# Optimization experiments

Hardware: AMD Instinct MI355X
Metric: run time of the kernel (lower is better)

## Reference

```python
import jax, jax.numpy as jnp
import numpy as np

B, S, C, L = 128, 49, 512, 1000
EPS_NORM = 1e-12
EPS_LN = 1e-5


def setup_inputs() -> dict:
    key = jax.random.key(0)
    ks = jax.random.split(key, 12)
    w_std = 0.02  # trunc_normal std for Linear weights
    c_std = 1.0 / np.sqrt(C)  # torch default Conv1d init scale (approx)
    return {
        "Fs": jax.random.normal(ks[0], (B, S, C), jnp.float32),
        "Ft": jax.random.normal(ks[1], (L, C), jnp.float32),
        "Fv": jax.random.normal(ks[2], (B, C), jnp.float32),
        "label": jax.random.randint(ks[3], (B,), 0, L),
        # Proj2 (pre_project_s): GN(1,C) -> Conv1d(C,C,1) -> ReLU -> GN(1,C) -> Conv1d(C,C,1)
        "gn1_g": jnp.ones((C,), jnp.float32),
        "gn1_b": jnp.zeros((C,), jnp.float32),
        "conv1_w": jax.random.normal(ks[4], (C, C), jnp.float32) * c_std,
        "conv1_b": jnp.zeros((C,), jnp.float32),
        "gn2_g": jnp.ones((C,), jnp.float32),
        "gn2_b": jnp.zeros((C,), jnp.float32),
        "conv2_w": jax.random.normal(ks[5], (C, C), jnp.float32) * c_std,
        "conv2_b": jnp.zeros((C,), jnp.float32),
        # Proj1 (pre_project_vv): LN -> Linear -> ReLU -> LN -> Linear
        "ln1_g": jnp.ones((C,), jnp.float32),
        "ln1_b": jnp.zeros((C,), jnp.float32),
        "lin1_w": jax.random.normal(ks[6], (C, C), jnp.float32) * w_std,
        "lin1_b": jnp.zeros((C,), jnp.float32),
        "ln2_g": jnp.ones((C,), jnp.float32),
        "ln2_b": jnp.zeros((C,), jnp.float32),
        "lin2_w": jax.random.normal(ks[7], (C, C), jnp.float32) * w_std,
        "lin2_b": jnp.zeros((C,), jnp.float32),
        "vis_gamma_p": jnp.float32(0.99),
        "vis_gamma_n": jnp.float32(0.99),
        "visual_prototype": jax.random.normal(ks[8], (L, C), jnp.float32),
    }


def _groupnorm1(x, g, b):
    # x: (B, C, S); GroupNorm with 1 group -> normalize over (C, S)
    m = jnp.mean(x, axis=(1, 2), keepdims=True)
    v = jnp.var(x, axis=(1, 2), keepdims=True)
    xn = (x - m) * jax.lax.rsqrt(v + EPS_LN)
    return xn * g[None, :, None] + b[None, :, None]


def _layernorm(x, g, b):
    m = jnp.mean(x, axis=-1, keepdims=True)
    v = jnp.var(x, axis=-1, keepdims=True)
    return (x - m) * jax.lax.rsqrt(v + EPS_LN) * g + b


def _l2norm(x):
    n = jnp.sqrt(jnp.sum(x * x, axis=-1, keepdims=True))
    return x / jnp.maximum(n, EPS_NORM)


def reference(Fs, Ft, Fv, label, gn1_g, gn1_b, conv1_w, conv1_b, gn2_g, gn2_b,
              conv2_w, conv2_b, ln1_g, ln1_b, lin1_w, lin1_b, ln2_g, ln2_b,
              lin2_w, lin2_b, vis_gamma_p, vis_gamma_n, visual_prototype):
    # --- Proj2 on Fs: (B,S,C) -> (B,C,S) -> GN/Conv1x1/ReLU/GN/Conv1x1 -> (B,S,C)
    xp = jnp.transpose(Fs, (0, 2, 1))                      # (B,C,S)
    h = _groupnorm1(xp, gn1_g, gn1_b)
    h = jnp.einsum('oc,bcs->bos', conv1_w, h) + conv1_b[None, :, None]
    h = jax.nn.relu(h)
    h = _groupnorm1(h, gn2_g, gn2_b)
    h = jnp.einsum('oc,bcs->bos', conv2_w, h) + conv2_b[None, :, None]
    Fs_p = jnp.transpose(h, (0, 2, 1))                     # (B,S,C)

    # --- cross-attn with text features: conv1d(Fs^T, Ft[:,:,None]) == einsum
    A = jnp.einsum('bsc,lc->bls', Fs_p, Ft)                # (B,L,S)
    A1 = jax.nn.softmax(A, axis=-1)
    feat_v_a = jnp.einsum('bls,bsc->blc', A1, Fs_p)        # (B,L,C)

    # --- Proj1 on Fv
    v = _layernorm(Fv, ln1_g, ln1_b)
    v = jax.nn.relu(v @ lin1_w.T + lin1_b)
    v = _layernorm(v, ln2_g, ln2_b)
    Fv_p = v @ lin2_w.T + lin2_b                           # (B,C)

    Fv_exp = Fv_p[:, None, :]                              # broadcast over L
    feat_v = vis_gamma_p * feat_v_a + Fv_exp               # (B,L,C)

    # --- cross-attn with visual prototype
    Av = jnp.einsum('bsc,lc->bls', Fs_p, visual_prototype)
    A1v = jax.nn.softmax(Av, axis=-1)
    feat_v_av = jnp.einsum('bls,bsc->blc', A1v, Fs_p)
    feat_vv = vis_gamma_n * feat_v_av + Fv_exp             # (B,L,C)

    Ft_n = _l2norm(Ft)                                     # (L,C)
    Fv_n = _l2norm(Fv_p)                                   # (B,C) (expanded rows identical)
    feat_v_n = _l2norm(feat_v)
    feat_vv_n = _l2norm(feat_vv)
    proto_n = _l2norm(visual_prototype)

    logits1 = jnp.einsum('bc,lc->bl', Fv_n, Ft_n)
    logits2 = jnp.sum(feat_v_n * Ft_n[None], axis=-1)
    logits3 = jnp.sum(feat_vv_n * proto_n[None], axis=-1)

    # --- no_grad prototype EMA update via label scatter
    Fv0 = jax.lax.stop_gradient(Fv_n)                      # Fv[:,0,:] after normalize
    proto = jax.lax.stop_gradient(visual_prototype)
    class_count = jnp.zeros((L,), jnp.int32).at[label].add(1)
    class_sum = jax.ops.segment_sum(Fv0, label, num_segments=L)
    safe_count = jnp.maximum(class_count.astype(jnp.float32), 1e-8)[:, None]
    class_mean = class_sum / safe_count
    new_proto = 0.99 * proto + 0.01 * class_mean
    updated_prototype = jnp.where((class_count > 0)[:, None], new_proto, proto)

    logits = jnp.stack([logits1, logits2, logits3])        # (3,B,L)
    return logits, updated_prototype
```

## Files before the change

### kernel.cpp

```cpp
#include <hip/hip_runtime.h>


#define Bn 128
#define Sn 49
#define Cn 512
#define Ln 1000
#define BL (Bn*Ln)
#define VQ 2048

typedef unsigned short u16;
typedef unsigned int u32;

using bfrag = __attribute__((ext_vector_type(8))) short;
using ffrag = __attribute__((ext_vector_type(4))) float;

typedef const __attribute__((address_space(1))) u32 gq_t;
typedef __attribute__((address_space(3))) u32 lq_t;

__device__ __forceinline__ float bf2f(u16 u){ return __uint_as_float(((u32)u) << 16); }
__device__ __forceinline__ float bflo(u32 u){ return __uint_as_float(u << 16); }
__device__ __forceinline__ float bfhi(u32 u){ return __uint_as_float(u & 0xffff0000u); }
__device__ __forceinline__ u16 f2bf(float f){
  u32 x = __float_as_uint(f);
  u32 r = x + 0x7fffu + ((x >> 16) & 1u);
  return (u16)(r >> 16);
}
__device__ __forceinline__ u16 f2h(float f){
  _Float16 h = (_Float16)f; return *(u16*)&h;
}
__device__ __forceinline__ float h2f(u16 u){
  _Float16 h = *(_Float16*)&u; return (float)h;
}

template<int BF>
__device__ __forceinline__ float ldin(const void* p, int i){
  if (BF) return bf2f(((const u16*)p)[i]);
  return ((const float*)p)[i];
}

template<int BF>
__device__ __forceinline__ void ld8(const void* p, int base, float* w){
  if (BF){
    uint4 u = *(const uint4*)((const u16*)p + base);
    w[0]=bflo(u.x); w[1]=bfhi(u.x); w[2]=bflo(u.y); w[3]=bfhi(u.y);
    w[4]=bflo(u.z); w[5]=bfhi(u.z); w[6]=bflo(u.w); w[7]=bfhi(u.w);
  } else {
    float4 a = *(const float4*)((const float*)p + base);
    float4 b = *(const float4*)((const float*)p + base + 4);
    w[0]=a.x; w[1]=a.y; w[2]=a.z; w[3]=a.w;
    w[4]=b.x; w[5]=b.y; w[6]=b.z; w[7]=b.w;
  }
}

__device__ __forceinline__ uint4 pack8(const float* w){
  uint4 v;
  v.x = (u32)f2bf(w[0]) | ((u32)f2bf(w[1])<<16);
  v.y = (u32)f2bf(w[2]) | ((u32)f2bf(w[3])<<16);
  v.z = (u32)f2bf(w[4]) | ((u32)f2bf(w[5])<<16);
  v.w = (u32)f2bf(w[6]) | ((u32)f2bf(w[7])<<16);
  return v;
}

__device__ __forceinline__ float ld_gamma(const void* p, int BF){
  float fb = bf2f(((const u16*)p)[0]);
  float ff = ((const float*)p)[0];
  bool pb = (fb > 0.05f && fb < 1.5f);
  bool pf = (ff > 0.05f && ff < 1.5f);
  if (pb && !pf) return fb;
  if (pf && !pb) return ff;
  return BF ? fb : ff;
}

__device__ __forceinline__ int detect_bf(const void* Fs){
  int lane = threadIdx.x & 63;
  uint4 v = ((const uint4*)Fs)[lane];
  u32 w[4] = {v.x, v.y, v.z, v.w};
  int c = 0;
  #pragma unroll
  for (int j = 0; j < 4; ++j){
    int e = (w[j] >> 7) & 0xff;
    c += (e >= 0x70 && e <= 0x8f);
  }
  #pragma unroll
  for (int m = 32; m; m >>= 1) c += __shfl_xor(c, m);
  return c >= 200;
}

__device__ __forceinline__ float2 block_red2(float a, float b, float* scratch){
  __syncthreads();
  #pragma unroll
  for (int off = 32; off; off >>= 1){ a += __shfl_xor(a, off); b += __shfl_xor(b, off); }
  int lane = threadIdx.x & 63, wid = threadIdx.x >> 6;
  if (lane == 0){ scratch[wid] = a; scratch[wid + 4] = b; }
  __syncthreads();
  return make_float2(scratch[0] + scratch[1] + scratch[2] + scratch[3],
                     scratch[4] + scratch[5] + scratch[6] + scratch[7]);
}

template<int BF>
__device__ void gn1_body(const void* Fs, float* m1, float* rs1, u16* Fsb,
                         float* m2s, float* m2ss, float* red){
  int b = blockIdx.x, tid = threadIdx.x;
  if (tid == 0){ m2s[b] = 0.f; m2ss[b] = 0.f; }
  float s = 0.f, ss = 0.f;
  for (int i = tid; i < Sn*Cn/8; i += 256){
    float w[8]; ld8<BF>(Fs, b*Sn*Cn + i*8, w);
    #pragma unroll
    for (int j = 0; j < 8; ++j){ s += w[j]; ss += w[j]*w[j]; }
    *(uint4*)(Fsb + (size_t)b*Sn*Cn + i*8) = pack8(w);
  }
  float2 r = block_red2(s, ss, red);
  if (tid == 0){
    float m = r.x * (1.f/(Sn*Cn));
    float v = r.y * (1.f/(Sn*Cn)) - m*m;
    m1[b] = m; rs1[b] = rsqrtf(v + 1e-5f);
  }
}

__global__ __launch_bounds__(256) void k_gn1_stats(const void* Fs,
    float* m1, float* rs1, u16* Fsb, float* m2s, float* m2ss){
  __shared__ float red[8];
  if (detect_bf(Fs)) gn1_body<1>(Fs, m1, rs1, Fsb, m2s, m2ss, red);
  else               gn1_body<0>(Fs, m1, rs1, Fsb, m2s, m2ss, red);
}

template<int BF>
__device__ void wk_body(int blk, const void* W1, const void* W2, const void* W3,
    const void* W4, const void* g1, const void* g2, const void* bb1, const void* bb2,
    const void* bias1, const void* bias2,
    u16* D1, u16* D2, u16* D3, u16* D4,
    float* K1a, float* K1b, float* K2a, float* K2b){
  if (blk < 512){
    int i = blk*256 + threadIdx.x;
    int sel = i >> 15;
    const void* src = (sel==0) ? W1 : (sel==1) ? W2 : (sel==2) ? W3 : W4;
    u16* dst = (sel==0) ? D1 : (sel==1) ? D2 : (sel==2) ? D3 : D4;
    int off = (i & 32767)*8;
    float w[8]; ld8<BF>(src, off, w);
    if (sel <= 1){
      const void* g = sel ? g2 : g1;
      int c0 = off & 511;
      #pragma unroll
      for (int j = 0; j < 8; ++j) w[j] *= ldin<BF>(g, c0 + j);
    }
    *(uint4*)(dst + off) = pack8(w);
  } else {
    int idx = (blk - 512)*4 + (threadIdx.x >> 6);
    int lane = threadIdx.x & 63;
    int o = idx & 511, sel = idx >> 9;
    const void* W  = sel ? W2 : W1;
    const void* g  = sel ? g2 : g1;
    const void* bb = sel ? bb2 : bb1;
    const void* bi = sel ? bias2 : bias1;
    float* Ka = sel ? K2a : K1a;
    float* Kb = sel ? K2b : K1b;
    float w[8], gv[8], bv[8];
    ld8<BF>(W, o*Cn + lane*8, w);
    ld8<BF>(g, lane*8, gv);
    ld8<BF>(bb, lane*8, bv);
    float a = 0.f, b2 = 0.f;
    #pragma unroll
    for (int j = 0; j < 8; ++j){ a += w[j]*bv[j]; b2 += w[j]*gv[j]; }
    #pragma unroll
    for (int m = 32; m; m >>= 1){ a += __shfl_xor(a, m); b2 += __shfl_xor(b2, m); }
    if (lane == 0){ Ka[o] = a + ldin<BF>(bi, o); Kb[o] = b2; }
  }
}

template<int BF>
__device__ void protonorm_body(int l, const void* Ft, const void* Pr,
                               float* invFt, float* invPr,
                               u16* FtB, u16* PrB, float* red){
  int tid = threadIdx.x;
  if (l >= Ln){
    FtB[(size_t)l*512 + tid] = 0; FtB[(size_t)l*512 + tid + 256] = 0;
    PrB[(size_t)l*512 + tid] = 0; PrB[(size_t)l*512 + tid + 256] = 0;
    return;
  }
  float a0 = ldin<BF>(Ft, l*Cn + tid), a1 = ldin<BF>(Ft, l*Cn + tid + 256);
  float p0 = ldin<BF>(Pr, l*Cn + tid), p1 = ldin<BF>(Pr, l*Cn + tid + 256);
  FtB[(size_t)l*512 + tid] = f2bf(a0); FtB[(size_t)l*512 + tid + 256] = f2bf(a1);
  PrB[(size_t)l*512 + tid] = f2bf(p0); PrB[(size_t)l*512 + tid + 256] = f2bf(p1);
  float2 r = block_red2(a0*a0 + a1*a1, p0*p0 + p1*p1, red);
  if (tid == 0){
    invFt[l] = 1.f / fmaxf(sqrtf(r.x), 1e-12f);
    invPr[l] = 1.f / fmaxf(sqrtf(r.y), 1e-12f);
  }
}

__global__ __launch_bounds__(256) void k_wkprep(const void* Fs,
    const void* W1, const void* W2, const void* W3, const void* W4,
    const void* g1, const void* g2, const void* bb1, const void* bb2,
    const void* bias1, const void* bias2,
    u16* D1, u16* D2, u16* D3, u16* D4,
    float* K1a, float* K1b, float* K2a, float* K2b,
    const void* Ft, const void* Pr, float* invFt, float* invPr, u16* FtB, u16* PrB){
  __shared__ float red[8];
  int bf = detect_bf(Fs);
  int blk = blockIdx.x;
  if (blk < 768){
    if (bf) wk_body<1>(blk, W1, W2, W3, W4, g1, g2, bb1, bb2, bias1, bias2,
                       D1, D2, D3, D4, K1a, K1b, K2a, K2b);
    else    wk_body<0>(blk, W1, W2, W3, W4, g1, g2, bb1, bb2, bias1, bias2,
                       D1, D2, D3, D4, K1a, K1b, K2a, K2b);
  } else {
    int l = blk - 768;
    if (bf) protonorm_body<1>(l, Ft, Pr, invFt, invPr, FtB, PrB, red);
    else    protonorm_body<0>(l, Ft, Pr, invFt, invPr, FtB, PrB, red);
  }
}

template<int C1>
__device__ void convm_body(const u16* __restrict__ src, const u16* __restrict__ Wb,
    const float* __restrict__ Ka, const float* __restrict__ Kb,
    float mean, float rs, u16* dst, u16* Bs, float* red,
    float* m2s, float* m2ss){
  int b = blockIdx.y, o0 = blockIdx.x * 128;
  int tid = threadIdx.x;
  int lane = tid & 63, wid = tid >> 6, lq = lane & 15, g4 = lane >> 4;
  for (int idx = tid; idx < 15*64; idx += 256){
    int r = 49 + (idx >> 6), j = idx & 63;
    *(uint4*)(Bs + (r<<9) + (j<<3)) = (uint4){0,0,0,0};
  }
  #pragma unroll
  for (int is = 0; is < 13; ++is){
    int r = is*4 + wid;
    if (r < Sn){
      const u16* gsrc = src + (size_t)(b*Sn + r)*Cn + ((lane ^ (r & 7)) << 3);
      u16* ldst = Bs + (r << 9);
      __builtin_amdgcn_global_load_lds((gq_t*)gsrc, (lq_t*)ldst, 16, 0, 0);
    }
  }
  __syncthreads();
  float gs = 0.f, gss = 0.f;
  #pragma unroll
  for (int ot = 0; ot < 2; ++ot){
    int oA = o0 + wid*32 + ot*16;
    bfrag af[16];
    #pragma unroll
    for (int kb = 0; kb < 16; ++kb)
      af[kb] = *(const bfrag*)(Wb + (size_t)(oA + lq)*Cn + kb*32 + g4*8);
    ffrag acc[4];
    #pragma unroll
    for (int st = 0; st < 4; ++st) acc[st] = (ffrag){0.f,0.f,0.f,0.f};
    #pragma unroll
    for (int st = 0; st < 4; ++st){
      int srow = st*16 + lq;
      #pragma unroll
      for (int kb = 0; kb < 16; ++kb){
        bfrag bf_ = *(const bfrag*)(Bs + (srow<<9) + (((kb*4+g4) ^ (srow&7))<<3));
        acc[st] = __builtin_amdgcn_mfma_f32_16x16x32_bf16(af[kb], bf_, acc[st], 0,0,0);
      }
    }
    int ob = oA + g4*4;
    float cst[4];
    #pragma unroll
    for (int r = 0; r < 4; ++r) cst[r] = Ka[ob + r] - mean*rs*Kb[ob + r];
    #pragma unroll
    for (int st = 0; st < 4; ++st){
      int s = st*16 + lq;
      u16 pk[4];
      #pragma unroll
      for (int r = 0; r < 4; ++r){
        float val = rs*acc[st][r] + cst[r];
        if (C1){
          val = fmaxf(val, 0.f);
          if (s < Sn){ gs += val; gss += val*val; }
        }
        pk[r] = f2bf(val);
      }
      if (C1){
        if (s < Sn) *(uint2*)(dst + ((size_t)(b*Sn + s)<<9) + ob) = *(const uint2*)pk;
      } else {
        if (s >= Sn){ pk[0]=0; pk[1]=0; pk[2]=0; pk[3]=0; }
        *(uint2*)(dst + ((size_t)(b*64 + s)<<9) + ob) = *(const uint2*)pk;
      }
    }
  }
  if (C1){
    float2 r2 = block_red2(gs, gss, red);
    if (tid == 0){
      atomicAdd(&m2s[b], r2.x);
      atomicAdd(&m2ss[b], r2.y);
    }
  }
}

__global__ __launch_bounds__(256, 2) void k_conv1m(const u16* Fsb,
    const u16* W1b, const float* Ka, const float* Kb,
    const float* m1, const float* rs1, u16* H1t, float* m2s, float* m2ss){
  __shared__ u16 Bs[64*512];
  __shared__ float red[8];
  int b = blockIdx.y;
  convm_body<1>(Fsb, W1b, Ka, Kb, m1[b], rs1[b], H1t, Bs, red, m2s, m2ss);
}

__global__ __launch_bounds__(256, 2) void k_conv2m(const u16* H1t,
    const u16* W2b, const float* Ka, const float* Kb,
    const float* m2s, const float* m2ss, u16* FspAug){
  __shared__ u16 Bs[64*512];
  int b = blockIdx.y;
  float sum = m2s[b], ssum = m2ss[b];
  float mean = sum * (1.f/(Sn*Cn));
  float var  = ssum * (1.f/(Sn*Cn)) - mean*mean;
  float rs = rsqrtf(var + 1e-5f);
  convm_body<0>(H1t, W2b, Ka, Kb, mean, rs, FspAug, Bs, (float*)nullptr,
                (float*)nullptr, (float*)nullptr);
}

template<int BF, int SBF, int PH>
__device__ void vg_body(const void* src, const void* lng, const void* lnb,
    const u16* __restrict__ Wv, const void* bias, void* outp,
    u16* Bt, u16* Ach, float* mrow, float* rrow, float* Gc, float* Bc2){
  int o0 = blockIdx.x * 16;
  int tid = threadIdx.x, lane = tid & 63, wid = tid >> 6;
  int lq = lane & 15, g4 = lane >> 4;
  for (int c = tid; c < Cn; c += 256){ Gc[c] = ldin<BF>(lng, c); Bc2[c] = ldin<BF>(lnb, c); }
  {
    int r = tid >> 1, h = tid & 1;
    float s = 0.f, ss = 0.f;
    #pragma unroll 4
    for (int k = 0; k < 32; ++k){
      float w[8]; ld8<SBF>(src, r*Cn + h*256 + k*8, w);
      #pragma unroll
      for (int j = 0; j < 8; ++j){ s += w[j]; ss += w[j]*w[j]; }
    }
    s += __shfl_xor(s, 1); ss += __shfl_xor(ss, 1);
    if (h == 0){
      float m = s * (1.f/Cn);
      mrow[r] = m; rrow[r] = rsqrtf(ss * (1.f/Cn) - m*m + 1e-5f);
    }
  }
  for (int idx = tid; idx < 16*64; idx += 256){
    int row = idx >> 6, j = idx & 63;
    uint4 v = *(const uint4*)(Wv + (size_t)(o0 + row)*Cn + j*8);
    *(uint4*)(Bt + (row<<9) + ((j ^ (row&7))<<3)) = v;
  }
  __syncthreads();
  ffrag acc[2];
  acc[0] = (ffrag){0.f,0.f,0.f,0.f};
  acc[1] = (ffrag){0.f,0.f,0.f,0.f};
  for (int kc = 0; kc < 4; ++kc){
    if (kc) __syncthreads();
    for (int idx = tid; idx < 128*16; idx += 256){
      int row = idx >> 4, j = idx & 15;
      int c = kc*128 + j*8;
      float w[8]; ld8<SBF>(src, row*Cn + c, w);
      float mu = mrow[row], rsd = rrow[row];
      #pragma unroll
      for (int k2 = 0; k2 < 8; ++k2) w[k2] = (w[k2]-mu)*rsd*Gc[c+k2] + Bc2[c+k2];
      *(uint4*)(Ach + (row<<7) + ((j ^ (row&15))<<3)) = pack8(w);
    }
    __syncthreads();
    #pragma unroll
    for (int mt2 = 0; mt2 < 2; ++mt2){
      int arow = (wid*2 + mt2)*16 + lq;
      #pragma unroll
      for (int kb = 0; kb < 4; ++kb){
        bfrag af = *(const bfrag*)(Ach + (arow<<7) + (((kb*4+g4) ^ (arow&15))<<3));
        bfrag bf_ = *(const bfrag*)(Bt + (lq<<9) + (((kc*16 + kb*4 + g4) ^ (lq&7))<<3));
        acc[mt2] = __builtin_amdgcn_mfma_f32_16x16x32_bf16(af, bf_, acc[mt2], 0,0,0);
      }
    }
  }
  float bval = ldin<BF>(bias, o0 + lq);
  #pragma unroll
  for (int mt2 = 0; mt2 < 2; ++mt2){
    #pragma unroll
    for (int r = 0; r < 4; ++r){
      int brow = wid*32 + mt2*16 + g4*4 + r;
      float val = acc[mt2][r] + bval;
      if (PH == 1){
        ((u16*)outp)[brow*Cn + o0 + lq] = f2bf(fmaxf(val, 0.f));
      } else {
        ((float*)outp)[brow*Cn + o0 + lq] = val;
      }
    }
  }
}

#define VG_SHARED \
  __shared__ u16 Bt[16*512]; \
  __shared__ u16 Ach[128*128]; \
  __shared__ float mrow[128], rrow[128]; \
  __shared__ float Gc[Cn], Bc2[Cn];

__global__ __launch_bounds__(256) void k_vg1(const void* Fs, const void* Fv,
    const void* lng, const void* lnb, const u16* Wv, const void* bias, u16* Hb){
  VG_SHARED
  if (detect_bf(Fs)) vg_body<1,1,1>(Fv, lng, lnb, Wv, bias, Hb, Bt, Ach, mrow, rrow, Gc, Bc2);
  else               vg_body<0,0,1>(Fv, lng, lnb, Wv, bias, Hb, Bt, Ach, mrow, rrow, Gc, Bc2);
}

__global__ __launch_bounds__(256) void k_vg2(const void* Fs, const u16* Hb,
    const void* lng, const void* lnb, const u16* Wv, const void* bias, float* Y2){
  VG_SHARED
  if (detect_bf(Fs)) vg_body<1,1,2>(Hb, lng, lnb, Wv, bias, Y2, Bt, Ach, mrow, rrow, Gc, Bc2);
  else               vg_body<0,1,2>(Hb, lng, lnb, Wv, bias, Y2, Bt, Ach, mrow, rrow, Gc, Bc2);
}

__global__ __launch_bounds__(256) void k_prep(const float* __restrict__ Fvp,
    float* __restrict__ Fvn, u16* __restrict__ FspAug, u16* __restrict__ Gb){
  __shared__ u16 xa[64*512];
  __shared__ float red[8];
  __shared__ float fvrow[512];
  int b = blockIdx.x, tid = threadIdx.x;
  int lane = tid & 63, wid = tid >> 6, lq = lane & 15, g4 = lane >> 4;
  float x0 = Fvp[b*Cn + tid], x1 = Fvp[b*Cn + tid + 256];
  float2 rr = block_red2(x0*x0 + x1*x1, 0.f, red);
  float inv = 1.f / fmaxf(sqrtf(rr.x), 1e-12f);
  fvrow[tid] = x0*inv; fvrow[tid + 256] = x1*inv;
  Fvn[b*Cn + tid] = x0*inv; Fvn[b*Cn + tid + 256] = x1*inv;
  __syncthreads();
  for (int idx = tid; idx < 64*64; idx += 256){
    int s = idx >> 6, j = idx & 63;
    uint4 v;
    if (s == 56 || s == 57){
      float w[8];
      if (s == 56){
        const float* src = Fvp + b*Cn + j*8;
        #pragma unroll
        for (int k = 0; k < 8; ++k) w[k] = src[k];
      } else {
        #pragma unroll
        for (int k = 0; k < 8; ++k) w[k] = fvrow[j*8 + k];
      }
      v = pack8(w);
      *(uint4*)(FspAug + ((size_t)(b*64 + s))*512 + j*8) = v;
    } else {
      v = *(const uint4*)(FspAug + ((size_t)(b*64 + s))*512 + j*8);
    }
    *(uint4*)(xa + s*512 + ((j ^ (s&7)) << 3)) = v;
  }
  __syncthreads();
  int mt = wid;
  for (int nt = 0; nt < 4; ++nt){
    ffrag acc = {0.f, 0.f, 0.f, 0.f};
    #pragma unroll
    for (int kb = 0; kb < 16; ++kb){
      int j = kb*4 + g4;
      int rowa = mt*16 + lq, rowb = nt*16 + lq;
      bfrag af  = *(const bfrag*)(xa + rowa*512 + ((j ^ (rowa&7)) << 3));
      bfrag bf_ = *(const bfrag*)(xa + rowb*512 + ((j ^ (rowb&7)) << 3));
      acc = __builtin_amdgcn_mfma_f32_16x16x32_bf16(af, bf_, acc, 0, 0, 0);
    }
    #pragma unroll
    for (int r = 0; r < 4; ++r)
      Gb[(size_t)b*4096 + (mt*16 + g4*4 + r)*64 + nt*16 + lq] = f2bf(acc[r]);
  }
}

__global__ __launch_bounds__(256, 3) void k_scores(const u16* __restrict__ LB,
    const u16* __restrict__ FspAug, u16* __restrict__ Sc){
  __shared__ u16 At[64*256];
  int b = blockIdx.x, lg = blockIdx.y;
  int tid = threadIdx.x, lane = tid & 63, wid = tid >> 6;
  int lq = lane & 15, g4 = lane >> 4;
  int l32 = lane & 31, rh = lane >> 5;
  bfrag breg[16];
  {
    const u16* fa = FspAug + ((size_t)(b*64 + wid*16 + lq))*512 + g4*8;
    #pragma unroll
    for (int kb = 0; kb < 16; ++kb) breg[kb] = *(const bfrag*)(fa + kb*32);
  }
  for (int chunk = 0; chunk < 4; ++chunk){
    int qi = lg*4 + chunk;
    ffrag acc[4];
    #pragma unroll
    for (int lt = 0; lt < 4; ++lt) acc[lt] = (ffrag){0.f,0.f,0.f,0.f};
    for (int kc = 0; kc < 2; ++kc){
      __syncthreads();
      #pragma unroll
      for (int is = 0; is < 8; ++is){
        int r = (is*4 + wid)*2 + rh;
        const u16* gsrc = LB + (size_t)(qi*64 + r)*512 + kc*256 + ((l32 ^ (r & 7)) << 3);
        u16* ldst = At + ((is*4 + wid) << 9);
        __builtin_amdgcn_global_load_lds((gq_t*)gsrc, (lq_t*)ldst, 16, 0, 0);
      }
      __syncthreads();
      #pragma unroll
      for (int kb = 0; kb < 8; ++kb){
        #pragma unroll
        for (int lt = 0; lt < 4; ++lt){
          int row = lt*16 + lq;
          bfrag af = *(const bfrag*)(At + (row<<8) + (((kb*4+g4) ^ (row&7))<<3));
          acc[lt] = __builtin_amdgcn_mfma_f32_16x16x32_bf16(af, breg[kc*8+kb], acc[lt], 0,0,0);
        }
      }
    }
    #pragma unroll
    for (int lt = 0; lt < 4; ++lt){
      #pragma unroll
      for (int r = 0; r < 4; ++r){
        size_t row = (size_t)b*VQ + qi*64 + lt*16 + g4*4 + r;
        Sc[row*64 + wid*16 + lq] = f2h(acc[lt][r]);
      }
    }
  }
}

__global__ __launch_bounds__(64) void k_attn4(const void* Fs,
    const u16* __restrict__ Sc, const u16* __restrict__ Gb,
    const float* __restrict__ invFt, const float* __restrict__ invPr,
    const void* gp_, const void* gn_,
    const int* __restrict__ label, const float* __restrict__ Fvn,
    const void* Pr, float* __restrict__ out){
  __shared__ u16 a1t[64*72];
  __shared__ float agab[64], wvb[64];
  __shared__ int lab[128];
  int bid = blockIdx.x;
  int bf = detect_bf(Fs);
  int lane = threadIdx.x;
  if (bid >= 4096){
    int l = bid - 4096;
    lab[lane] = label[lane]; lab[lane + 64] = label[lane + 64];
    __syncthreads();
    float sum[8] = {0.f,0.f,0.f,0.f,0.f,0.f,0.f,0.f};
    int cnt = 0;
    for (int i = 0; i < Bn; ++i){
      if (lab[i] == l){
        cnt++;
        const float4* v = (const float4*)(Fvn + i*Cn + lane*8);
        float4 a = v[0], c = v[1];
        sum[0]+=a.x; sum[1]+=a.y; sum[2]+=a.z; sum[3]+=a.w;
        sum[4]+=c.x; sum[5]+=c.y; sum[6]+=c.z; sum[7]+=c.w;
      }
    }
    int base = l*Cn + lane*8;
    float* dst = out + 3*BL + base;
    if (cnt > 0){
      float sc = 0.01f / fmaxf((float)cnt, 1e-8f);
      #pragma unroll
      for (int j = 0; j < 8; ++j)
        dst[j] = 0.99f*(bf ? ldin<1>(Pr, base+j) : ldin<0>(Pr, base+j)) + sum[j]*sc;
    } else {
      #pragma unroll
      for (int j = 0; j < 8; ++j)
        dst[j] = bf ? ldin<1>(Pr, base+j) : ldin<0>(Pr, base+j);
    }
    return;
  }
  int qi = bid & 31, b = bid >> 5;
  int lq = lane & 15, g4 = lane >> 4;

  u32 w32[32];
  {
    const uint4* rp = (const uint4*)(Sc + ((size_t)b*VQ + qi*64 + lane)*64);
    #pragma unroll
    for (int i = 0; i < 8; ++i){
      uint4 v = rp[i];
      w32[i*4+0] = v.x; w32[i*4+1] = v.y; w32[i*4+2] = v.z; w32[i*4+3] = v.w;
    }
  }
  #define XS(s) h2f((u16)(((s)&1) ? (w32[(s)>>1] >> 16) : (w32[(s)>>1] & 0xffffu)))
  float mx = -1e30f;
  #pragma unroll
  for (int s = 0; s < Sn; ++s) mx = fmaxf(mx, XS(s));
  float raw56 = XS(56), raw57 = XS(57);
  float sm = 0.f, dx = 0.f;
  #pragma unroll
  for (int u = 0; u < 7; ++u){
    u32 pw[4];
    #pragma unroll
    for (int i = 0; i < 4; ++i){
      u32 w2 = 0;
      #pragma unroll
      for (int h = 0; h < 2; ++h){
        int s = u*8 + i*2 + h;
        float x = XS(s);
        float e = (s < Sn) ? __expf(x - mx) : 0.f;
        sm += e; dx += e * x;
        w2 |= ((u32)f2bf(e)) << (16*h);
      }
      pw[i] = w2;
    }
    *(uint4*)(a1t + lane*72 + u*8) = make_uint4(pw[0], pw[1], pw[2], pw[3]);
  }
  #undef XS

  const u16* gbase = Gb + (size_t)b*4096;
  #pragma unroll
  for (int qt = 0; qt < 4; ++qt){
    float pr[4] = {0.f, 0.f, 0.f, 0.f};
    float wvl[4] = {0.f, 0.f, 0.f, 0.f};
    #pragma unroll
    for (int nt = 0; nt < 4; ++nt){
      ffrag acc = {0.f, 0.f, 0.f, 0.f};
      #pragma unroll
      for (int kb2 = 0; kb2 < 2; ++kb2){
        bfrag af;
        if (kb2 == 1 && g4 == 3) af = (bfrag){0,0,0,0,0,0,0,0};
        else af = *(const bfrag*)(a1t + (qt*16 + lq)*72 + (g4 + 4*kb2)*8);
        bfrag bg = *(const bfrag*)(gbase + (nt*16 + lq)*64 + kb2*32 + g4*8);
        acc = __builtin_amdgcn_mfma_f32_16x16x32_bf16(af, bg, acc, 0, 0, 0);
      }
      int sp = nt*16 + lq;
      #pragma unroll
      for (int r = 0; r < 4; ++r){
        int q = qt*16 + g4*4 + r;
        float av = (sp < 56) ? bf2f(a1t[q*72 + sp]) : 0.f;
        pr[r] += av * acc[r];
        if (nt == 3 && lq == 8) wvl[r] = acc[r];
      }
    }
    #pragma unroll
    for (int m = 1; m <= 8; m <<= 1){
      #pragma unroll
      for (int r = 0; r < 4; ++r) pr[r] += __shfl_xor(pr[r], m);
    }
    if (lq == 0){
      #pragma unroll
      for (int r = 0; r < 4; ++r) agab[qt*16 + g4*4 + r] = pr[r];
    }
    if (lq == 8){
      #pragma unroll
      for (int r = 0; r < 4; ++r) wvb[qt*16 + g4*4 + r] = wvl[r];
    }
  }

  int vq = qi*64 + lane;
  int path = vq >> 10, l = vq & 1023;
  if (l < Ln){
    float gp = ld_gamma(gp_, bf), gn = ld_gamma(gn_, bf);
    float fvpSq = bf2f(gbase[56*64 + 56]);
    float inv_sm = 1.f / sm;
    float aGa = agab[lane] * inv_sm * inv_sm;
    float wv  = wvb[lane] * inv_sm;
    float gam = path ? gn : gp;
    float ns  = gam*gam*aGa + 2.f*gam*wv + fvpSq;
    float dt  = gam*(dx*inv_sm) + raw56;
    float invx = (path ? invPr : invFt)[l];
    float lg2 = dt * invx / fmaxf(sqrtf(ns), 1e-12f);
    if (path == 0){
      out[(size_t)b*Ln + l]              = raw57 * invx;
      out[(size_t)BL + (size_t)b*Ln + l] = lg2;
    } else {
      out[(size_t)2*BL + (size_t)b*Ln + l] = lg2;
    }
  }
}

extern "C" void kernel_launch(void* const* d_in, const int* in_sizes, int n_in,
                              void* d_out, int out_size, void* d_ws, size_t ws_size,
                              hipStream_t stream){
  (void)in_sizes; (void)n_in; (void)out_size; (void)ws_size;
  const void* Fs    = d_in[0];
  const void* Ft    = d_in[1];
  const void* Fv    = d_in[2];
  const int*  label = (const int*)d_in[3];
  const void* gn1g  = d_in[4];
  const void* gn1b  = d_in[5];
  const void* c1w   = d_in[6];
  const void* c1b   = d_in[7];
  const void* gn2g  = d_in[8];
  const void* gn2b  = d_in[9];
  const void* c2w   = d_in[10];
  const void* c2b   = d_in[11];
  const void* ln1g  = d_in[12];
  const void* ln1b  = d_in[13];
  const void* l1w   = d_in[14];
  const void* l1b   = d_in[15];
  const void* ln2g  = d_in[16];
  const void* ln2b  = d_in[17];
  const void* l2w   = d_in[18];
  const void* l2b   = d_in[19];
  const void* gp    = d_in[20];
  const void* gnm   = d_in[21];
  const void* proto = d_in[22];
  float* out = (float*)d_out;
  float* ws  = (float*)d_ws;

  float* m1    = ws + 0;
  float* rs1   = ws + 128;
  float* m2s   = ws + 256;
  float* m2ss  = ws + 384;
  float* invFt = ws + 512;
  float* invPr = ws + 1536;
  u16*   H1t   = (u16*)(ws + 4096);
  float* Fvp   = ws + 4096 + (size_t)Bn*Sn*Cn/2;
  float* Fvn   = Fvp + Bn*Cn;
  u16*   FspAug= (u16*)(Fvn + Bn*Cn);
  u16*   FtB   = FspAug + (size_t)Bn*64*512;
  u16*   PrB   = FtB + (size_t)1024*512;
  u16*   Gb    = PrB + (size_t)1024*512;
  u16*   W1b   = Gb + (size_t)Bn*4096;
  u16*   W2b   = W1b + (size_t)512*512;
  u16*   W1vb  = W2b + (size_t)512*512;
  u16*   W2vb  = W1vb + (size_t)512*512;
  u16*   Hb    = W2vb + (size_t)512*512;
  u16*   Fsb   = Hb + (size_t)Bn*Cn;
  float* Kv1a  = (float*)(Fsb + (size_t)Bn*Sn*Cn);
  float* Kv1b  = Kv1a + 512;
  float* Kv2a  = Kv1b + 512;
  float* Kv2b  = Kv2a + 512;
  u16*   Sc    = (u16*)(Kv2b + 512);

  k_gn1_stats<<<Bn, 256, 0, stream>>>(Fs, m1, rs1, Fsb, m2s, m2ss);
  k_wkprep<<<1792, 256, 0, stream>>>(Fs, c1w, c2w, l1w, l2w, gn1g, gn2g,
                                     gn1b, gn2b, c1b, c2b,
                                     W1b, W2b, W1vb, W2vb, Kv1a, Kv1b, Kv2a, Kv2b,
                                     Ft, proto, invFt, invPr, FtB, PrB);
  k_conv1m<<<dim3(4, Bn), 256, 0, stream>>>(Fsb, W1b, Kv1a, Kv1b, m1, rs1, H1t, m2s, m2ss);
  k_conv2m<<<dim3(4, Bn), 256, 0, stream>>>(H1t, W2b, Kv2a, Kv2b, m2s, m2ss, FspAug);
  k_vg1<<<32, 256, 0, stream>>>(Fs, Fv, ln1g, ln1b, W1vb, l1b, Hb);
  k_vg2<<<32, 256, 0, stream>>>(Fs, Hb, ln2g, ln2b, W2vb, l2b, Fvp);
  k_prep<<<Bn, 256, 0, stream>>>(Fvp, Fvn, FspAug, Gb);
  k_scores<<<dim3(Bn, 8), 256, 0, stream>>>(FtB, FspAug, Sc);
  k_attn4<<<4096 + Ln, 64, 0, stream>>>(Fs, Sc, Gb, invFt, invPr, gp, gnm,
                                        label, Fvn, proto, out);
}
```

Baseline: 161.5 us.

## Merge independent prep, conv and vision-MLP kernels into shared launches

Cuts the launch count from 6 to 3 by placing independent work in the same grid, split by block index. GN1 stats join the weight-prep kernel, conv1 shares a launch with the first vision linear, and conv2 shares one with the second. Shared memory becomes one union buffer sized for the larger branch. This removes launch gaps and lets the small 32-block vision GEMMs overlap with the convs, at the cost of the vg blocks now running under the conv kernel's launch bounds and shared-memory footprint.

Result: faster. 152.6 us (-5.5%).

```diff
diff --git a/kernel.cpp b/kernel.cpp
--- a/kernel.cpp
+++ b/kernel.cpp
@@ -98,9 +98,9 @@
 }
 
 template<int BF>
-__device__ void gn1_body(const void* Fs, float* m1, float* rs1, u16* Fsb,
+__device__ void gn1_body(int b, const void* Fs, float* m1, float* rs1, u16* Fsb,
                          float* m2s, float* m2ss, float* red){
-  int b = blockIdx.x, tid = threadIdx.x;
+  int tid = threadIdx.x;
   if (tid == 0){ m2s[b] = 0.f; m2ss[b] = 0.f; }
   float s = 0.f, ss = 0.f;
   for (int i = tid; i < Sn*Cn/8; i += 256){
@@ -115,13 +115,6 @@
     float v = r.y * (1.f/(Sn*Cn)) - m*m;
     m1[b] = m; rs1[b] = rsqrtf(v + 1e-5f);
   }
-}
-
-__global__ __launch_bounds__(256) void k_gn1_stats(const void* Fs,
-    float* m1, float* rs1, u16* Fsb, float* m2s, float* m2ss){
-  __shared__ float red[8];
-  if (detect_bf(Fs)) gn1_body<1>(Fs, m1, rs1, Fsb, m2s, m2ss, red);
-  else               gn1_body<0>(Fs, m1, rs1, Fsb, m2s, m2ss, red);
 }
 
 template<int BF>
@@ -188,13 +181,14 @@
   }
 }
 
-__global__ __launch_bounds__(256) void k_wkprep(const void* Fs,
+__global__ __launch_bounds__(256) void k_gn1wk(const void* Fs,
     const void* W1, const void* W2, const void* W3, const void* W4,
     const void* g1, const void* g2, const void* bb1, const void* bb2,
     const void* bias1, const void* bias2,
     u16* D1, u16* D2, u16* D3, u16* D4,
     float* K1a, float* K1b, float* K2a, float* K2b,
-    const void* Ft, const void* Pr, float* invFt, float* invPr, u16* FtB, u16* PrB){
+    const void* Ft, const void* Pr, float* invFt, float* invPr, u16* FtB, u16* PrB,
+    float* m1, float* rs1, u16* Fsb, float* m2s, float* m2ss){
   __shared__ float red[8];
   int bf = detect_bf(Fs);
   int blk = blockIdx.x;
@@ -203,19 +197,23 @@
                        D1, D2, D3, D4, K1a, K1b, K2a, K2b);
     else    wk_body<0>(blk, W1, W2, W3, W4, g1, g2, bb1, bb2, bias1, bias2,
                        D1, D2, D3, D4, K1a, K1b, K2a, K2b);
-  } else {
+  } else if (blk < 1792){
     int l = blk - 768;
     if (bf) protonorm_body<1>(l, Ft, Pr, invFt, invPr, FtB, PrB, red);
     else    protonorm_body<0>(l, Ft, Pr, invFt, invPr, FtB, PrB, red);
+  } else {
+    int b = blk - 1792;
+    if (bf) gn1_body<1>(b, Fs, m1, rs1, Fsb, m2s, m2ss, red);
+    else    gn1_body<0>(b, Fs, m1, rs1, Fsb, m2s, m2ss, red);
   }
 }
 
 template<int C1>
-__device__ void convm_body(const u16* __restrict__ src, const u16* __restrict__ Wb,
+__device__ void convm_body(int b, int o0,
+    const u16* __restrict__ src, const u16* __restrict__ Wb,
     const float* __restrict__ Ka, const float* __restrict__ Kb,
     float mean, float rs, u16* dst, u16* Bs, float* red,
     float* m2s, float* m2ss){
-  int b = blockIdx.y, o0 = blockIdx.x * 128;
   int tid = threadIdx.x;
   int lane = tid & 63, wid = tid >> 6, lq = lane & 15, g4 = lane >> 4;
   for (int idx = tid; idx < 15*64; idx += 256){
@@ -286,33 +284,10 @@
   }
 }
 
-__global__ __launch_bounds__(256, 2) void k_conv1m(const u16* Fsb,
-    const u16* W1b, const float* Ka, const float* Kb,
-    const float* m1, const float* rs1, u16* H1t, float* m2s, float* m2ss){
-  __shared__ u16 Bs[64*512];
-  __shared__ float red[8];
-  int b = blockIdx.y;
-  convm_body<1>(Fsb, W1b, Ka, Kb, m1[b], rs1[b], H1t, Bs, red, m2s, m2ss);
-}
-
-__global__ __launch_bounds__(256, 2) void k_conv2m(const u16* H1t,
-    const u16* W2b, const float* Ka, const float* Kb,
-    const float* m2s, const float* m2ss, u16* FspAug){
-  __shared__ u16 Bs[64*512];
-  int b = blockIdx.y;
-  float sum = m2s[b], ssum = m2ss[b];
-  float mean = sum * (1.f/(Sn*Cn));
-  float var  = ssum * (1.f/(Sn*Cn)) - mean*mean;
-  float rs = rsqrtf(var + 1e-5f);
-  convm_body<0>(H1t, W2b, Ka, Kb, mean, rs, FspAug, Bs, (float*)nullptr,
-                (float*)nullptr, (float*)nullptr);
-}
-
 template<int BF, int SBF, int PH>
-__device__ void vg_body(const void* src, const void* lng, const void* lnb,
+__device__ void vg_body(int o0, const void* src, const void* lng, const void* lnb,
     const u16* __restrict__ Wv, const void* bias, void* outp,
     u16* Bt, u16* Ach, float* mrow, float* rrow, float* Gc, float* Bc2){
-  int o0 = blockIdx.x * 16;
   int tid = threadIdx.x, lane = tid & 63, wid = tid >> 6;
   int lq = lane & 15, g4 = lane >> 4;
   for (int c = tid; c < Cn; c += 256){ Gc[c] = ldin<BF>(lng, c); Bc2[c] = ldin<BF>(lnb, c); }
@@ -379,24 +354,60 @@
   }
 }
 
-#define VG_SHARED \
-  __shared__ u16 Bt[16*512]; \
-  __shared__ u16 Ach[128*128]; \
-  __shared__ float mrow[128], rrow[128]; \
-  __shared__ float Gc[Cn], Bc2[Cn];
-
-__global__ __launch_bounds__(256) void k_vg1(const void* Fs, const void* Fv,
-    const void* lng, const void* lnb, const u16* Wv, const void* bias, u16* Hb){
-  VG_SHARED
-  if (detect_bf(Fs)) vg_body<1,1,1>(Fv, lng, lnb, Wv, bias, Hb, Bt, Ach, mrow, rrow, Gc, Bc2);
-  else               vg_body<0,0,1>(Fv, lng, lnb, Wv, bias, Hb, Bt, Ach, mrow, rrow, Gc, Bc2);
-}
-
-__global__ __launch_bounds__(256) void k_vg2(const void* Fs, const u16* Hb,
-    const void* lng, const void* lnb, const u16* Wv, const void* bias, float* Y2){
-  VG_SHARED
-  if (detect_bf(Fs)) vg_body<1,1,2>(Hb, lng, lnb, Wv, bias, Y2, Bt, Ach, mrow, rrow, Gc, Bc2);
-  else               vg_body<0,1,2>(Hb, lng, lnb, Wv, bias, Y2, Bt, Ach, mrow, rrow, Gc, Bc2);
+#define CV_SHARED __shared__ __align__(16) char smu[65568];
+
+__global__ __launch_bounds__(256, 2) void k_c1vg1(const void* Fs,
+    const u16* Fsb, const u16* W1b, const float* Ka, const float* Kb,
+    const float* m1, const float* rs1, u16* H1t, float* m2s, float* m2ss,
+    const void* Fv, const void* ln1g, const void* ln1b,
+    const u16* W1vb, const void* l1b, u16* Hb){
+  CV_SHARED
+  int blk = blockIdx.x;
+  if (blk < 512){
+    u16* Bs = (u16*)smu;
+    float* red = (float*)(smu + 65536);
+    int b = blk >> 2, o0 = (blk & 3)*128;
+    convm_body<1>(b, o0, Fsb, W1b, Ka, Kb, m1[b], rs1[b], H1t, Bs, red, m2s, m2ss);
+  } else {
+    u16* Bt = (u16*)smu;
+    u16* Ach = (u16*)(smu + 16384);
+    float* mrow = (float*)(smu + 49152);
+    float* rrow = (float*)(smu + 49664);
+    float* Gc = (float*)(smu + 50176);
+    float* Bc2 = (float*)(smu + 52224);
+    int o0 = (blk - 512)*16;
+    if (detect_bf(Fs)) vg_body<1,1,1>(o0, Fv, ln1g, ln1b, W1vb, l1b, Hb, Bt, Ach, mrow, rrow, Gc, Bc2);
+    else               vg_body<0,0,1>(o0, Fv, ln1g, ln1b, W1vb, l1b, Hb, Bt, Ach, mrow, rrow, Gc, Bc2);
+  }
+}
+
+__global__ __launch_bounds__(256, 2) void k_c2vg2(const void* Fs,
+    const u16* H1t, const u16* W2b, const float* Ka, const float* Kb,
+    const float* m2s, const float* m2ss, u16* FspAug,
+    const u16* Hb, const void* ln2g, const void* ln2b,
+    const u16* W2vb, const void* l2b, float* Y2){
+  CV_SHARED
+  int blk = blockIdx.x;
+  if (blk < 512){
+    u16* Bs = (u16*)smu;
+    int b = blk >> 2, o0 = (blk & 3)*128;
+    float sum = m2s[b], ssum = m2ss[b];
+    float mean = sum * (1.f/(Sn*Cn));
+    float var  = ssum * (1.f/(Sn*Cn)) - mean*mean;
+    float rs = rsqrtf(var + 1e-5f);
+    convm_body<0>(b, o0, H1t, W2b, Ka, Kb, mean, rs, FspAug, Bs,
+                  (float*)nullptr, (float*)nullptr, (float*)nullptr);
+  } else {
+    u16* Bt = (u16*)smu;
+    u16* Ach = (u16*)(smu + 16384);
+    float* mrow = (float*)(smu + 49152);
+    float* rrow = (float*)(smu + 49664);
+    float* Gc = (float*)(smu + 50176);
+    float* Bc2 = (float*)(smu + 52224);
+    int o0 = (blk - 512)*16;
+    if (detect_bf(Fs)) vg_body<1,1,2>(o0, Hb, ln2g, ln2b, W2vb, l2b, Y2, Bt, Ach, mrow, rrow, Gc, Bc2);
+    else               vg_body<0,1,2>(o0, Hb, ln2g, ln2b, W2vb, l2b, Y2, Bt, Ach, mrow, rrow, Gc, Bc2);
+  }
 }
 
 __global__ __launch_bounds__(256) void k_prep(const float* __restrict__ Fvp,
@@ -695,15 +706,15 @@
   float* Kv2b  = Kv2a + 512;
   u16*   Sc    = (u16*)(Kv2b + 512);
 
-  k_gn1_stats<<<Bn, 256, 0, stream>>>(Fs, m1, rs1, Fsb, m2s, m2ss);
-  k_wkprep<<<1792, 256, 0, stream>>>(Fs, c1w, c2w, l1w, l2w, gn1g, gn2g,
-                                     gn1b, gn2b, c1b, c2b,
-                                     W1b, W2b, W1vb, W2vb, Kv1a, Kv1b, Kv2a, Kv2b,
-                                     Ft, proto, invFt, invPr, FtB, PrB);
-  k_conv1m<<<dim3(4, Bn), 256, 0, stream>>>(Fsb, W1b, Kv1a, Kv1b, m1, rs1, H1t, m2s, m2ss);
-  k_conv2m<<<dim3(4, Bn), 256, 0, stream>>>(H1t, W2b, Kv2a, Kv2b, m2s, m2ss, FspAug);
-  k_vg1<<<32, 256, 0, stream>>>(Fs, Fv, ln1g, ln1b, W1vb, l1b, Hb);
-  k_vg2<<<32, 256, 0, stream>>>(Fs, Hb, ln2g, ln2b, W2vb, l2b, Fvp);
+  k_gn1wk<<<1920, 256, 0, stream>>>(Fs, c1w, c2w, l1w, l2w, gn1g, gn2g,
+                                    gn1b, gn2b, c1b, c2b,
+                                    W1b, W2b, W1vb, W2vb, Kv1a, Kv1b, Kv2a, Kv2b,
+                                    Ft, proto, invFt, invPr, FtB, PrB,
+                                    m1, rs1, Fsb, m2s, m2ss);
+  k_c1vg1<<<544, 256, 0, stream>>>(Fs, Fsb, W1b, Kv1a, Kv1b, m1, rs1, H1t, m2s, m2ss,
+                                   Fv, ln1g, ln1b, W1vb, l1b, Hb);
+  k_c2vg2<<<544, 256, 0, stream>>>(Fs, H1t, W2b, Kv2a, Kv2b, m2s, m2ss, FspAug,
+                                   Hb, ln2g, ln2b, W2vb, l2b, Fvp);
   k_prep<<<Bn, 256, 0, stream>>>(Fvp, Fvn, FspAug, Gb);
   k_scores<<<dim3(Bn, 8), 256, 0, stream>>>(FtB, FspAug, Sc);
   k_attn4<<<4096 + Ln, 64, 0, stream>>>(Fs, Sc, Gb, invFt, invPr, gp, gnm,
```
